# Kernel optimization log

Hardware: AMD Instinct MI355X
Metric: run time of the kernel (lower is better)

The kernel has to match this reference:

```python
import jax, jax.numpy as jnp
import numpy as np

N = 100000
E = 3200000
D_IN = 83
D_HID = 1024
N_CLASSES = 25


def setup_inputs() -> dict:
    key = jax.random.key(0)
    ks = jax.random.split(key, 10)
    feature = jax.random.normal(ks[0], (N, D_IN), dtype=jnp.float32)
    edge_row = jax.random.randint(ks[1], (E,), 0, N, dtype=jnp.int32)
    edge_col = jax.random.randint(ks[2], (E,), 0, N, dtype=jnp.int32)
    adj_val = jax.random.uniform(ks[3], (E,), dtype=jnp.float32)
    # Conv1d(1 -> 4, kernel 5, pad 2): weight [out=4, in=1, k=5]
    conv_w = jax.random.normal(ks[4], (4, 1, 5), dtype=jnp.float32) * 0.2
    conv_b = jnp.zeros((4,), dtype=jnp.float32)
    # GCN weights (kaiming-uniform-like scale), zero biases
    W1 = jax.random.uniform(ks[5], (D_IN, D_HID), dtype=jnp.float32,
                            minval=-1.0, maxval=1.0) * np.sqrt(6.0 / D_IN)
    b1 = jnp.zeros((D_HID,), dtype=jnp.float32)
    W2 = jax.random.uniform(ks[6], (D_HID, N_CLASSES), dtype=jnp.float32,
                            minval=-1.0, maxval=1.0) * np.sqrt(6.0 / D_HID)
    b2 = jnp.zeros((N_CLASSES,), dtype=jnp.float32)
    return {"feature": feature, "conv_w": conv_w, "conv_b": conv_b,
            "W1": W1, "b1": b1, "W2": W2, "b2": b2,
            "adj_val": adj_val, "edge_row": edge_row, "edge_col": edge_col}


def _spmm(vals, row, col, X):
    # sparse(adj) @ X : gather source rows, scale by edge value, scatter-add to dest
    return jax.ops.segment_sum(vals[:, None] * X[col], row, num_segments=N)


def reference(feature, conv_w, conv_b, W1, b1, W2, b2, adj_val, edge_row, edge_col):
    # Conv1d prelude: [N,1,83] -> [N,4,83], sum over channels, relu -> [N,83]
    x = jax.lax.conv_general_dilated(
        feature[:, None, :], conv_w, window_strides=(1,), padding=[(2, 2)],
        dimension_numbers=("NCH", "OIH", "NCH"))
    x = x + conv_b[None, :, None]
    x = jax.nn.relu(jnp.sum(x, axis=1))
    # GCN layer 1: relu(A @ (x W1) + b1)
    h = jax.nn.relu(_spmm(adj_val, edge_row, edge_col, x @ W1) + b1)
    # GCN layer 2: A @ (h W2) + b2
    logits = _spmm(adj_val, edge_row, edge_col, h @ W2) + b2
    return logits
```

## Files before the change

### kernel.cpp

```cpp
#include <hip/hip_runtime.h>

#define NN   100000
#define EE   3200000
#define DIN  83
#define DHID 1024
#define NCLS 25
#define XPAD 96
#define ZPAD 32

#define NBK     391
#define SLAB    10240
#define CHUNK   8192

typedef __attribute__((__ext_vector_type__(8))) short sh8;
typedef __attribute__((__ext_vector_type__(4))) float f4_t;

static __device__ __forceinline__ float relu_(float v) { return v > 0.f ? v : 0.f; }

static __device__ __forceinline__ unsigned short f2bf(float f) {
  unsigned int u = __float_as_uint(f);
  unsigned int r = u + 0x7FFFu + ((u >> 16) & 1u);
  return (unsigned short)(r >> 16);
}
static __device__ __forceinline__ float bflo(unsigned int q) {
  return __uint_as_float(q << 16);
}
static __device__ __forceinline__ float bfhi(unsigned int q) {
  return __uint_as_float(q & 0xFFFF0000u);
}

__global__ __launch_bounds__(256) void prelude_k(
    const float* __restrict__ feature, const float* __restrict__ conv_w,
    const float* __restrict__ conv_b, unsigned short* __restrict__ x,
    const float* __restrict__ W1, unsigned short* __restrict__ w1t,
    const float* __restrict__ W2, unsigned short* __restrict__ w2t,
    int* __restrict__ gcur) {
  const int tid = threadIdx.x;
  int t = blockIdx.x * 256 + tid;
  if (t < DHID * XPAD) {
    int k = t / DHID;
    int n = t - k * DHID;
    float v = (k < DIN) ? W1[k * DHID + n] : 0.f;
    w1t[n * XPAD + k] = f2bf(v);
  }
  if (t < 32 * DHID) {
    int k = t / 32;
    int n = t - k * 32;
    float v = (n < NCLS) ? W2[k * NCLS + n] : 0.f;
    w2t[n * DHID + k] = f2bf(v);
  }
  if (t < NBK * 16) gcur[t] = 0;
  const int nb0 = blockIdx.x * 16;
  if (nb0 >= NN) return;
  __shared__ float fs[16 * 84];
  const size_t base = (size_t)nb0 * DIN;
  for (int i = tid; i < 16 * DIN; i += 256) {
    int nl = i / DIN;
    int dd = i - nl * DIN;
    fs[nl * 84 + dd] = feature[base + i];
  }
  __syncthreads();
  if (tid >= 192) return;
  int nl = tid / 12;
  int g = tid - nl * 12;
  int i0 = g * 8;
  float ws0 = conv_w[0] + conv_w[5] + conv_w[10] + conv_w[15];
  float ws1 = conv_w[1] + conv_w[6] + conv_w[11] + conv_w[16];
  float ws2 = conv_w[2] + conv_w[7] + conv_w[12] + conv_w[17];
  float ws3 = conv_w[3] + conv_w[8] + conv_w[13] + conv_w[18];
  float ws4 = conv_w[4] + conv_w[9] + conv_w[14] + conv_w[19];
  float bs  = conv_b[0] + conv_b[1] + conv_b[2] + conv_b[3];
  const float* f = &fs[nl * 84];
  float fv[12];
#pragma unroll
  for (int k = 0; k < 12; ++k) {
    int idx = i0 - 2 + k;
    fv[k] = (idx >= 0 && idx < DIN) ? f[idx] : 0.f;
  }
  sh8 vout;
#pragma unroll
  for (int j = 0; j < 8; ++j) {
    int i = i0 + j;
    unsigned short o = 0;
    if (i < DIN) {
      float acc = bs + ws0 * fv[j] + ws1 * fv[j + 1] + ws2 * fv[j + 2] +
                  ws3 * fv[j + 3] + ws4 * fv[j + 4];
      o = f2bf(relu_(acc));
    }
    vout[j] = (short)o;
  }
  *(sh8*)&x[(size_t)(nb0 + nl) * XPAD + i0] = vout;
}

__global__ __launch_bounds__(512) void partition_k(
    const float* __restrict__ vals, const int* __restrict__ row,
    const int* __restrict__ col, int* __restrict__ gcur,
    int2* __restrict__ tmp) {
  __shared__ int cnt[NBK];
  __shared__ int lcur[NBK];
  const int tid = threadIdx.x;
  const int cb = blockIdx.x * CHUNK;
  const int csize = (cb + CHUNK <= EE) ? CHUNK : (EE - cb);

  for (int b = tid; b < NBK; b += 512) cnt[b] = 0;
  __syncthreads();
  for (int i = tid; i < csize; i += 512)
    atomicAdd(&cnt[row[cb + i] >> 8], 1);
  __syncthreads();
  for (int b = tid; b < NBK; b += 512)
    lcur[b] = cnt[b] ? (b * SLAB + atomicAdd(&gcur[b * 16], cnt[b])) : 0;
  __syncthreads();
  for (int i = tid; i < csize; i += 512) {
    int r = row[cb + i];
    int pos = atomicAdd(&lcur[r >> 8], 1);
    tmp[pos] = make_int2(col[cb + i] | ((r & 255) << 17),
                         __float_as_int(vals[cb + i]));
  }
}

__global__ __launch_bounds__(512) void fine_scatter2_k(
    const int* __restrict__ gcur, const int2* __restrict__ tmp,
    int2* __restrict__ csr, int* __restrict__ offs, int* __restrict__ counts) {
  __shared__ int cnt[256];
  __shared__ int sd[256];
  __shared__ int lcur[256];
  const int tid = threadIdx.x;
  const int b = blockIdx.x;
  const int r0 = b * 256;
  const int gstart = b * SLAB;
  const int nedge = gcur[b * 16];
  if (tid < 256) cnt[tid] = 0;
  __syncthreads();
  for (int i = tid; i < nedge; i += 512)
    atomicAdd(&cnt[((unsigned)tmp[gstart + i].x) >> 17], 1);
  __syncthreads();
  int v = 0;
  if (tid < 256) { v = cnt[tid]; sd[tid] = v; }
  __syncthreads();
  for (int off = 1; off < 256; off <<= 1) {
    int add = (tid >= off && tid < 256) ? sd[tid - off] : 0;
    __syncthreads();
    if (tid < 256) sd[tid] += add;
    __syncthreads();
  }
  if (tid < 256) {
    int excl = gstart + sd[tid] - v;
    int r = r0 + tid;
    if (r < NN) {
      offs[r] = excl;
      counts[r] = v;
    }
    lcur[tid] = excl;
  }
  __syncthreads();
  for (int i = tid; i < nedge; i += 512) {
    int2 p = tmp[gstart + i];
    int rl = ((unsigned)p.x) >> 17;
    int pos = atomicAdd(&lcur[rl], 1);
    csr[pos] = make_int2(p.x & 0x1FFFF, p.y);
  }
}

__global__ __launch_bounds__(256) void spmm83_g(
    const int* __restrict__ offs, const int* __restrict__ cnt,
    const int2* __restrict__ csr, const unsigned short* __restrict__ x,
    unsigned short* __restrict__ ax) {
  int wave = (int)((blockIdx.x * blockDim.x + threadIdx.x) >> 6);
  int lane = threadIdx.x & 63;
  if (wave >= NN) return;
  int s = __builtin_amdgcn_readfirstlane(offs[wave]);
  int n = __builtin_amdgcn_readfirstlane(cnt[wave]);
  const bool act = lane < 48;
  const int d2 = lane * 2;
  float a0 = 0.f, a1 = 0.f;
  int i = 0;
  for (; i + 16 <= n; i += 16) {
    int2 p[16];
#pragma unroll
    for (int u = 0; u < 16; ++u) p[u] = csr[s + i + u];
    if (act) {
      unsigned int q[16];
#pragma unroll
      for (int u = 0; u < 16; ++u)
        q[u] = *(const unsigned int*)&x[(size_t)p[u].x * XPAD + d2];
#pragma unroll
      for (int u = 0; u < 16; ++u) {
        float v = __int_as_float(p[u].y);
        a0 += v * bflo(q[u]);
        a1 += v * bfhi(q[u]);
      }
    }
  }
  for (; i + 8 <= n; i += 8) {
    int2 p[8];
#pragma unroll
    for (int u = 0; u < 8; ++u) p[u] = csr[s + i + u];
    if (act) {
      unsigned int q[8];
#pragma unroll
      for (int u = 0; u < 8; ++u)
        q[u] = *(const unsigned int*)&x[(size_t)p[u].x * XPAD + d2];
#pragma unroll
      for (int u = 0; u < 8; ++u) {
        float v = __int_as_float(p[u].y);
        a0 += v * bflo(q[u]);
        a1 += v * bfhi(q[u]);
      }
    }
  }
  for (; i < n; ++i) {
    int2 p = csr[s + i];
    if (act) {
      unsigned int q = *(const unsigned int*)&x[(size_t)p.x * XPAD + d2];
      float v = __int_as_float(p.y);
      a0 += v * bflo(q);
      a1 += v * bfhi(q);
    }
  }
  if (act) {
    unsigned int o = (unsigned int)f2bf(a0) | ((unsigned int)f2bf(a1) << 16);
    *(unsigned int*)&ax[(size_t)wave * XPAD + d2] = o;
  }
}

__global__ __launch_bounds__(256) void spmm25_g(
    const int* __restrict__ offs, const int* __restrict__ cnt,
    const int2* __restrict__ csr, const unsigned short* __restrict__ zb,
    const float* __restrict__ b2, float* __restrict__ out) {
  int gw = (int)((blockIdx.x * blockDim.x + threadIdx.x) >> 6);
  int lane = threadIdx.x & 63;
  int sub = lane >> 4;
  int d2 = (lane & 15) * 2;
  int r = gw * 4 + sub;
  if (r >= NN) return;
  int s = offs[r];
  int n = cnt[r];
  float a0 = 0.f, a1 = 0.f;
  int i = 0;
  for (; i + 8 <= n; i += 8) {
    int2 p[8];
#pragma unroll
    for (int u = 0; u < 8; ++u) p[u] = csr[s + i + u];
    unsigned int q[8];
#pragma unroll
    for (int u = 0; u < 8; ++u)
      q[u] = *(const unsigned int*)&zb[(size_t)p[u].x * ZPAD + d2];
#pragma unroll
    for (int u = 0; u < 8; ++u) {
      float v = __int_as_float(p[u].y);
      a0 += v * bflo(q[u]);
      a1 += v * bfhi(q[u]);
    }
  }
  for (; i < n; ++i) {
    int2 p = csr[s + i];
    unsigned int q = *(const unsigned int*)&zb[(size_t)p.x * ZPAD + d2];
    float v = __int_as_float(p.y);
    a0 += v * bflo(q);
    a1 += v * bfhi(q);
  }
  if (d2 < NCLS)     out[(size_t)r * NCLS + d2]     = a0 + b2[d2];
  if (d2 + 1 < NCLS) out[(size_t)r * NCLS + d2 + 1] = a1 + b2[d2 + 1];
}

__global__ __launch_bounds__(256) void fused_mlp_mfma(
    const unsigned short* __restrict__ axg, const unsigned short* __restrict__ w1t,
    const float* __restrict__ b1, const unsigned short* __restrict__ w2t,
    unsigned short* __restrict__ zb) {
  __shared__ __align__(16) unsigned short axs[128 * 104];
  __shared__ __align__(16) unsigned short hs[128 * 136];
  __shared__ float b1s[DHID];
  const int tid = threadIdx.x;
  const int n0 = blockIdx.x * 128;

  for (int idx = tid; idx < 128 * 12; idx += 256) {
    int m = idx / 12;
    int c8 = idx - m * 12;
    int node = n0 + m;
    sh8 v = {0, 0, 0, 0, 0, 0, 0, 0};
    if (node < NN) v = *(const sh8*)&axg[(size_t)node * XPAD + c8 * 8];
    *(sh8*)&axs[m * 104 + c8 * 8] = v;
  }
  for (int i = tid; i < DHID; i += 256) b1s[i] = b1[i];
  __syncthreads();

  const int lane = tid & 63;
  const int w = tid >> 6;
  const int quad = lane >> 4;
  const int tn = lane & 15;
  const int mta = w;
  const int mtb = w + 4;

  sh8 a1[8][3];
#pragma unroll
  for (int mt = 0; mt < 8; ++mt)
#pragma unroll
    for (int kc = 0; kc < 3; ++kc)
      a1[mt][kc] = *(const sh8*)&axs[(mt * 16 + tn) * 104 + kc * 32 + quad * 8];

  f4_t za0 = {0.f, 0.f, 0.f, 0.f}, za1 = {0.f, 0.f, 0.f, 0.f};
  f4_t zb0 = {0.f, 0.f, 0.f, 0.f}, zb1 = {0.f, 0.f, 0.f, 0.f};

  for (int c = 0; c < 8; ++c) {
    const int cb = c * 128;
#pragma unroll
    for (int nti = 0; nti < 2; ++nti) {
      const int nt = w * 2 + nti;
      const int ng = cb + nt * 16 + tn;
      const unsigned short* wr = &w1t[(size_t)ng * XPAD + quad * 8];
      sh8 b0 = *(const sh8*)&wr[0];
      sh8 b1f = *(const sh8*)&wr[32];
      sh8 b2f = *(const sh8*)&wr[64];
      float bias = b1s[ng];
#pragma unroll
      for (int mt = 0; mt < 8; ++mt) {
        f4_t acc = {0.f, 0.f, 0.f, 0.f};
        acc = __builtin_amdgcn_mfma_f32_16x16x32_bf16(a1[mt][0], b0, acc, 0, 0, 0);
        acc = __builtin_amdgcn_mfma_f32_16x16x32_bf16(a1[mt][1], b1f, acc, 0, 0, 0);
        acc = __builtin_amdgcn_mfma_f32_16x16x32_bf16(a1[mt][2], b2f, acc, 0, 0, 0);
#pragma unroll
        for (int r = 0; r < 4; ++r) {
          float v = relu_(acc[r] + bias);
          hs[(mt * 16 + quad * 4 + r) * 136 + nt * 16 + tn] = f2bf(v);
        }
      }
    }
    __syncthreads();
#pragma unroll
    for (int kc = 0; kc < 4; ++kc) {
      sh8 bl = *(const sh8*)&w2t[(size_t)tn * DHID + cb + kc * 32 + quad * 8];
      sh8 bh = *(const sh8*)&w2t[(size_t)(16 + tn) * DHID + cb + kc * 32 + quad * 8];
      sh8 aa = *(const sh8*)&hs[(mta * 16 + tn) * 136 + kc * 32 + quad * 8];
      za0 = __builtin_amdgcn_mfma_f32_16x16x32_bf16(aa, bl, za0, 0, 0, 0);
      za1 = __builtin_amdgcn_mfma_f32_16x16x32_bf16(aa, bh, za1, 0, 0, 0);
      sh8 ab = *(const sh8*)&hs[(mtb * 16 + tn) * 136 + kc * 32 + quad * 8];
      zb0 = __builtin_amdgcn_mfma_f32_16x16x32_bf16(ab, bl, zb0, 0, 0, 0);
      zb1 = __builtin_amdgcn_mfma_f32_16x16x32_bf16(ab, bh, zb1, 0, 0, 0);
    }
    __syncthreads();
  }

#pragma unroll
  for (int r = 0; r < 4; ++r) {
    int na = n0 + mta * 16 + quad * 4 + r;
    if (na < NN) {
      zb[(size_t)na * ZPAD + tn]      = f2bf(za0[r]);
      zb[(size_t)na * ZPAD + 16 + tn] = f2bf(za1[r]);
    }
    int nb = n0 + mtb * 16 + quad * 4 + r;
    if (nb < NN) {
      zb[(size_t)nb * ZPAD + tn]      = f2bf(zb0[r]);
      zb[(size_t)nb * ZPAD + 16 + tn] = f2bf(zb1[r]);
    }
  }
}

extern "C" void kernel_launch(void* const* d_in, const int* in_sizes, int n_in,
                              void* d_out, int out_size, void* d_ws, size_t ws_size,
                              hipStream_t stream) {
  const float* feature = (const float*)d_in[0];
  const float* conv_w  = (const float*)d_in[1];
  const float* conv_b  = (const float*)d_in[2];
  const float* W1      = (const float*)d_in[3];
  const float* b1      = (const float*)d_in[4];
  const float* W2      = (const float*)d_in[5];
  const float* b2      = (const float*)d_in[6];
  const float* adj     = (const float*)d_in[7];
  const int*   erow    = (const int*)d_in[8];
  const int*   ecol    = (const int*)d_in[9];
  float* out = (float*)d_out;

  char* B = (char*)d_ws;
  size_t o = 0;
  auto alloc = [&](size_t bytes, size_t align) -> void* {
    o = (o + align - 1) & ~(align - 1);
    void* p = B + o;
    o += bytes;
    return p;
  };
  unsigned short* x    = (unsigned short*)alloc((size_t)NN * XPAD * 2, 16);
  unsigned short* ax   = (unsigned short*)alloc((size_t)NN * XPAD * 2, 16);
  unsigned short* zb   = (unsigned short*)alloc((size_t)NN * ZPAD * 2, 16);
  int*   counts  = (int*)alloc((size_t)NN * 4, 16);
  int*   offs    = (int*)alloc((size_t)NN * 4, 16);
  int*   gcur    = (int*)alloc((size_t)NBK * 16 * 4, 64);
  unsigned short* w1t = (unsigned short*)alloc((size_t)DHID * XPAD * 2, 16);
  unsigned short* w2t = (unsigned short*)alloc((size_t)32 * DHID * 2, 16);
  int2*  tmp     = (int2*)alloc((size_t)NBK * SLAB * 8, 16);
  int2*  csr     = (int2*)alloc((size_t)NBK * SLAB * 8, 16);

  const int nblk_prelude = (NN + 15) / 16;
  prelude_k<<<nblk_prelude, 256, 0, stream>>>(
      feature, conv_w, conv_b, x, W1, w1t, W2, w2t, gcur);
  partition_k<<<(EE + CHUNK - 1) / CHUNK, 512, 0, stream>>>(
      adj, erow, ecol, gcur, tmp);
  fine_scatter2_k<<<NBK, 512, 0, stream>>>(gcur, tmp, csr, offs, counts);
  spmm83_g<<<(NN + 3) / 4, 256, 0, stream>>>(offs, counts, csr, x, ax);
  fused_mlp_mfma<<<(NN + 127) / 128, 256, 0, stream>>>(ax, w1t, b1, w2t, zb);
  spmm25_g<<<(NN + 15) / 16, 256, 0, stream>>>(offs, counts, csr, zb, b2, out);
}
```

Measured before the change: 431.8 us.

## Merge edge partition and conv prelude into one launch; stage bucket edges in LDS

Combines the edge-partition kernel and the conv/weight-transpose prelude into a single horizontally fused launch. The first 391 blocks partition edges and the remaining blocks handle conv and weight packing, now at 32 nodes per 512-thread block. The gcur reset moves to a hipMemsetAsync so the partition blocks no longer depend on the prelude having run. fine_scatter2_k now copies each bucket's edges into a 72KB LDS buffer when they fit, so tmp is read from global once instead of twice, at the cost of lower occupancy from the large shared allocation.

```diff
diff --git a/kernel.cpp b/kernel.cpp
--- a/kernel.cpp
+++ b/kernel.cpp
@@ -11,6 +11,9 @@
 #define NBK     391
 #define SLAB    10240
 #define CHUNK   8192
+#define NPART   391
+#define NCONVB  3125
+#define EBUF    9216
 
 typedef __attribute__((__ext_vector_type__(8))) short sh8;
 typedef __attribute__((__ext_vector_type__(4))) float f4_t;
@@ -29,14 +32,41 @@
   return __uint_as_float(q & 0xFFFF0000u);
 }
 
-__global__ __launch_bounds__(256) void prelude_k(
+__global__ __launch_bounds__(512) void build_k(
+    const float* __restrict__ vals, const int* __restrict__ row,
+    const int* __restrict__ col, int* __restrict__ gcur,
+    int2* __restrict__ tmp,
     const float* __restrict__ feature, const float* __restrict__ conv_w,
     const float* __restrict__ conv_b, unsigned short* __restrict__ x,
     const float* __restrict__ W1, unsigned short* __restrict__ w1t,
-    const float* __restrict__ W2, unsigned short* __restrict__ w2t,
-    int* __restrict__ gcur) {
+    const float* __restrict__ W2, unsigned short* __restrict__ w2t) {
+  __shared__ __align__(16) int shm[32 * 84];
   const int tid = threadIdx.x;
-  int t = blockIdx.x * 256 + tid;
+
+  if (blockIdx.x < NPART) {
+    int* cnt  = shm;
+    int* lcur = shm + NBK;
+    const int cb = blockIdx.x * CHUNK;
+    const int csize = (cb + CHUNK <= EE) ? CHUNK : (EE - cb);
+    for (int b = tid; b < NBK; b += 512) cnt[b] = 0;
+    __syncthreads();
+    for (int i = tid; i < csize; i += 512)
+      atomicAdd(&cnt[row[cb + i] >> 8], 1);
+    __syncthreads();
+    for (int b = tid; b < NBK; b += 512)
+      lcur[b] = cnt[b] ? (b * SLAB + atomicAdd(&gcur[b * 16], cnt[b])) : 0;
+    __syncthreads();
+    for (int i = tid; i < csize; i += 512) {
+      int r = row[cb + i];
+      int pos = atomicAdd(&lcur[r >> 8], 1);
+      tmp[pos] = make_int2(col[cb + i] | ((r & 255) << 17),
+                           __float_as_int(vals[cb + i]));
+    }
+    return;
+  }
+
+  const int cbk = blockIdx.x - NPART;
+  int t = cbk * 512 + tid;
   if (t < DHID * XPAD) {
     int k = t / DHID;
     int n = t - k * DHID;
@@ -49,18 +79,17 @@
     float v = (n < NCLS) ? W2[k * NCLS + n] : 0.f;
     w2t[n * DHID + k] = f2bf(v);
   }
-  if (t < NBK * 16) gcur[t] = 0;
-  const int nb0 = blockIdx.x * 16;
+  const int nb0 = cbk * 32;
   if (nb0 >= NN) return;
-  __shared__ float fs[16 * 84];
+  float* fs = (float*)shm;
   const size_t base = (size_t)nb0 * DIN;
-  for (int i = tid; i < 16 * DIN; i += 256) {
+  for (int i = tid; i < 32 * DIN; i += 512) {
     int nl = i / DIN;
     int dd = i - nl * DIN;
     fs[nl * 84 + dd] = feature[base + i];
   }
   __syncthreads();
-  if (tid >= 192) return;
+  if (tid >= 384) return;
   int nl = tid / 12;
   int g = tid - nl * 12;
   int i0 = g * 8;
@@ -92,35 +121,10 @@
   *(sh8*)&x[(size_t)(nb0 + nl) * XPAD + i0] = vout;
 }
 
-__global__ __launch_bounds__(512) void partition_k(
-    const float* __restrict__ vals, const int* __restrict__ row,
-    const int* __restrict__ col, int* __restrict__ gcur,
-    int2* __restrict__ tmp) {
-  __shared__ int cnt[NBK];
-  __shared__ int lcur[NBK];
-  const int tid = threadIdx.x;
-  const int cb = blockIdx.x * CHUNK;
-  const int csize = (cb + CHUNK <= EE) ? CHUNK : (EE - cb);
-
-  for (int b = tid; b < NBK; b += 512) cnt[b] = 0;
-  __syncthreads();
-  for (int i = tid; i < csize; i += 512)
-    atomicAdd(&cnt[row[cb + i] >> 8], 1);
-  __syncthreads();
-  for (int b = tid; b < NBK; b += 512)
-    lcur[b] = cnt[b] ? (b * SLAB + atomicAdd(&gcur[b * 16], cnt[b])) : 0;
-  __syncthreads();
-  for (int i = tid; i < csize; i += 512) {
-    int r = row[cb + i];
-    int pos = atomicAdd(&lcur[r >> 8], 1);
-    tmp[pos] = make_int2(col[cb + i] | ((r & 255) << 17),
-                         __float_as_int(vals[cb + i]));
-  }
-}
-
 __global__ __launch_bounds__(512) void fine_scatter2_k(
     const int* __restrict__ gcur, const int2* __restrict__ tmp,
     int2* __restrict__ csr, int* __restrict__ offs, int* __restrict__ counts) {
+  __shared__ int2 ebuf[EBUF];
   __shared__ int cnt[256];
   __shared__ int sd[256];
   __shared__ int lcur[256];
@@ -129,10 +133,15 @@
   const int r0 = b * 256;
   const int gstart = b * SLAB;
   const int nedge = gcur[b * 16];
+  const bool fit = (nedge <= EBUF);
   if (tid < 256) cnt[tid] = 0;
-  __syncthreads();
-  for (int i = tid; i < nedge; i += 512)
-    atomicAdd(&cnt[((unsigned)tmp[gstart + i].x) >> 17], 1);
+  if (fit)
+    for (int i = tid; i < nedge; i += 512) ebuf[i] = tmp[gstart + i];
+  __syncthreads();
+  for (int i = tid; i < nedge; i += 512) {
+    int px = fit ? ebuf[i].x : tmp[gstart + i].x;
+    atomicAdd(&cnt[((unsigned)px) >> 17], 1);
+  }
   __syncthreads();
   int v = 0;
   if (tid < 256) { v = cnt[tid]; sd[tid] = v; }
@@ -154,7 +163,7 @@
   }
   __syncthreads();
   for (int i = tid; i < nedge; i += 512) {
-    int2 p = tmp[gstart + i];
+    int2 p = fit ? ebuf[i] : tmp[gstart + i];
     int rl = ((unsigned)p.x) >> 17;
     int pos = atomicAdd(&lcur[rl], 1);
     csr[pos] = make_int2(p.x & 0x1FFFF, p.y);
@@ -389,11 +398,10 @@
   int2*  tmp     = (int2*)alloc((size_t)NBK * SLAB * 8, 16);
   int2*  csr     = (int2*)alloc((size_t)NBK * SLAB * 8, 16);
 
-  const int nblk_prelude = (NN + 15) / 16;
-  prelude_k<<<nblk_prelude, 256, 0, stream>>>(
-      feature, conv_w, conv_b, x, W1, w1t, W2, w2t, gcur);
-  partition_k<<<(EE + CHUNK - 1) / CHUNK, 512, 0, stream>>>(
-      adj, erow, ecol, gcur, tmp);
+  hipMemsetAsync(gcur, 0, (size_t)NBK * 16 * 4, stream);
+  build_k<<<NPART + NCONVB, 512, 0, stream>>>(
+      adj, erow, ecol, gcur, tmp,
+      feature, conv_w, conv_b, x, W1, w1t, W2, w2t);
   fine_scatter2_k<<<NBK, 512, 0, stream>>>(gcur, tmp, csr, offs, counts);
   spmm83_g<<<(NN + 3) / 4, 256, 0, stream>>>(offs, counts, csr, x, ax);
   fused_mlp_mfma<<<(NN + 127) / 128, 256, 0, stream>>>(ax, w1t, b1, w2t, zb);
```

New measurement: 425.2 us. About the same (-1.5%).
